# Optimization experiments

Measured on AMD Instinct MI355X. Metric: run time of the kernel, lower is better.

Reference implementation:

```python
import jax, jax.numpy as jnp
import numpy as np

IN_F = 4096
OUT_F = 8192
BLOCK = 16   # block_dim
KEEP = 8     # keep_k low-frequency modes kept per block
NLEV = 256   # n_levels


def dct_inv_basis(keep_k, n):
    # Orthonormal DCT-II synthesis basis, rows = kept frequencies k, cols = time index t.
    k = jnp.arange(keep_k, dtype=jnp.float32)[:, None]
    t = jnp.arange(n, dtype=jnp.float32)[None, :]
    B = jnp.cos(jnp.pi * (t + 0.5) * k / n) * jnp.sqrt(2.0 / n)
    scale = jnp.where(jnp.arange(keep_k) == 0, 1.0 / jnp.sqrt(2.0), 1.0)
    return B * scale[:, None]  # [keep_k, block_dim]


def setup_inputs() -> dict:
    key = jax.random.key(0)
    k1, k2, k3, k4, k5 = jax.random.split(key, 5)
    n_blocks = OUT_F * IN_F // BLOCK  # 2097152
    x = jax.random.normal(k1, (32, 8, IN_F), jnp.float32)
    idx = jax.random.randint(k2, (n_blocks, KEEP), 0, NLEV, jnp.int32)
    c_min = jax.random.normal(k3, (KEEP,), jnp.float32)
    c_range = jax.random.uniform(k4, (KEEP,), jnp.float32) + 0.1
    bias = jax.random.normal(k5, (OUT_F,), jnp.float32)
    return {"x": x, "idx": idx, "c_min": c_min, "c_range": c_range, "bias": bias}


def reference(x, idx, c_min, c_range, bias):
    # Affine dequant of kept frequency codes: [n_blocks, keep_k]
    coeffs = idx.astype(jnp.float32) / (NLEV - 1) * c_range + c_min
    # Inverse DCT per block (high-frequency modes are implicitly zero)
    B = dct_inv_basis(KEEP, BLOCK)              # [keep_k, block_dim]
    W = (coeffs @ B).reshape(OUT_F, IN_F)       # dense dequantized weight
    return x @ W.T + bias
```

## Files before the change

### kernel.cpp

```cpp
#include <hip/hip_runtime.h>


typedef __attribute__((ext_vector_type(8))) short bf16x8;
typedef __attribute__((ext_vector_type(4))) float f32x4;

#define K_TOT  2048
#define N_TOT  8192
#define KSTEPS 64
#define DEPTH  4

__device__ __forceinline__ unsigned short f2bf_rn(float f) {
    unsigned u = __float_as_uint(f);
    u += 0x7FFFu + ((u >> 16) & 1u);
    return (unsigned short)(u >> 16);
}

__device__ __forceinline__ unsigned pack2(int a, int b) {
    unsigned ua = __float_as_uint((float)a);
    unsigned ub = __float_as_uint((float)b);
    return __builtin_amdgcn_perm(ub, ua, 0x07060302u);
}

__device__ __forceinline__ bf16x8 cvt_bfrag(int4 lo, int4 hi) {
    union { unsigned u[4]; bf16x8 v; } r;
    r.u[0] = pack2(lo.x, lo.y);
    r.u[1] = pack2(lo.z, lo.w);
    r.u[2] = pack2(hi.x, hi.y);
    r.u[3] = pack2(hi.z, hi.w);
    return r.v;
}

__global__ __launch_bounds__(256) void prep_kernel(
    const float* __restrict__ x, const float* __restrict__ c_min,
    const float* __restrict__ c_range, unsigned short* __restrict__ Y2f,
    float* __restrict__ corr)
{
    __shared__ float Bk[8][16];
    __shared__ float scmin[8];
    __shared__ float ss[8];
    __shared__ float red[4];
    const int tid = threadIdx.x;
    const int m = blockIdx.x;
    if (tid < 128) {
        int k = tid >> 4, t = tid & 15;
        float v = cosf(3.14159265358979f * (t + 0.5f) * (float)k / 16.0f)
                  * 0.353553390593274f;
        if (k == 0) v *= 0.707106781186548f;
        Bk[k][t] = v;
    }
    if (tid < 8) {
        scmin[tid] = c_min[tid];
        ss[tid] = c_range[tid] * (1.0f / 255.0f);
    }
    __syncthreads();

    const float* xp = x + (long)m * 4096 + tid * 16;
    float xs[16];
#pragma unroll
    for (int q = 0; q < 4; ++q) {
        float4 v = *(const float4*)(xp + q * 4);
        xs[q * 4 + 0] = v.x; xs[q * 4 + 1] = v.y;
        xs[q * 4 + 2] = v.z; xs[q * 4 + 3] = v.w;
    }
    float partial = 0.0f;
    unsigned short yo[8];
#pragma unroll
    for (int k = 0; k < 8; ++k) {
        float y = 0.0f;
#pragma unroll
        for (int t = 0; t < 16; ++t) y += xs[t] * Bk[k][t];
        partial += y * scmin[k];
        yo[k] = f2bf_rn(y * ss[k]);
    }
    uint4 pk;
    pk.x = (unsigned)yo[0] | ((unsigned)yo[1] << 16);
    pk.y = (unsigned)yo[2] | ((unsigned)yo[3] << 16);
    pk.z = (unsigned)yo[4] | ((unsigned)yo[5] << 16);
    pk.w = (unsigned)yo[6] | ((unsigned)yo[7] << 16);

    {
        const int mg = m >> 4, fr = m & 15, kc = tid >> 2, fq = tid & 3;
        unsigned short* dst = Y2f + ((long)((mg * 64 + kc) * 64) + fq * 16 + fr) * 8;
        *(uint4*)dst = pk;
    }

#pragma unroll
    for (int off = 32; off > 0; off >>= 1)
        partial += __shfl_down(partial, off, 64);
    if ((tid & 63) == 0) red[tid >> 6] = partial;
    __syncthreads();
    if (tid == 0) corr[m] = red[0] + red[1] + red[2] + red[3];
}

__global__ __launch_bounds__(256, 2) void gemm_kernel(
    const unsigned short* __restrict__ Y2f, const int* __restrict__ idx,
    const float* __restrict__ bias, const float* __restrict__ corr,
    float* __restrict__ out)
{
    const int tid  = threadIdx.x;
    const int wave = tid >> 6;
    const int lane = tid & 63;
    const int fr   = lane & 15;
    const int fq   = lane >> 4;
    const int o0   = blockIdx.x * 16;

    const int* bPtr = idx + (long)(o0 + fr) * K_TOT + fq * 8;
    const unsigned short* aPtr = Y2f + ((long)(wave * 4) * KSTEPS * 64 + lane) * 8;

    int4 bLo[DEPTH], bHi[DEPTH];
    bf16x8 aF[2][4];
    f32x4 acc[4] = {{0.f,0.f,0.f,0.f},{0.f,0.f,0.f,0.f},
                    {0.f,0.f,0.f,0.f},{0.f,0.f,0.f,0.f}};

#pragma unroll
    for (int s = 0; s < DEPTH; ++s) {
        const int* p = bPtr + s * 32;
        bLo[s] = *(const int4*)p;
        bHi[s] = *(const int4*)(p + 4);
    }
#pragma unroll
    for (int mt = 0; mt < 4; ++mt) {
        aF[0][mt] = *(const bf16x8*)(aPtr + mt * 32768);
        aF[1][mt] = *(const bf16x8*)(aPtr + mt * 32768 + 512);
    }

    for (int kc = 0; kc < KSTEPS; kc += DEPTH) {
#pragma unroll
        for (int u = 0; u < DEPTH; ++u) {
            const int k = kc + u;
            bf16x8 bf = cvt_bfrag(bLo[u], bHi[u]);
            if (k + DEPTH < KSTEPS) {
                const int* p = bPtr + (k + DEPTH) * 32;
                bLo[u] = *(const int4*)p;
                bHi[u] = *(const int4*)(p + 4);
            }
#pragma unroll
            for (int mt = 0; mt < 4; ++mt)
                acc[mt] = __builtin_amdgcn_mfma_f32_16x16x32_bf16(
                    aF[k & 1][mt], bf, acc[mt], 0, 0, 0);
            if (k + 2 < KSTEPS) {
#pragma unroll
                for (int mt = 0; mt < 4; ++mt)
                    aF[k & 1][mt] =
                        *(const bf16x8*)(aPtr + mt * 32768 + (k + 2) * 512);
            }
        }
    }

    const int col = o0 + fr;
    const float bv = bias[col];
#pragma unroll
    for (int mt = 0; mt < 4; ++mt) {
        const int row0 = wave * 64 + mt * 16 + fq * 4;
#pragma unroll
        for (int r = 0; r < 4; ++r)
            out[(long)(row0 + r) * N_TOT + col] = acc[mt][r] + bv + corr[row0 + r];
    }
}

extern "C" void kernel_launch(void* const* d_in, const int* in_sizes, int n_in,
                              void* d_out, int out_size, void* d_ws, size_t ws_size,
                              hipStream_t stream) {
    const float* x       = (const float*)d_in[0];
    const int*   idx     = (const int*)d_in[1];
    const float* c_min   = (const float*)d_in[2];
    const float* c_range = (const float*)d_in[3];
    const float* bias    = (const float*)d_in[4];
    float* out = (float*)d_out;

    unsigned short* Y2f = (unsigned short*)d_ws;
    float* corr = (float*)((char*)d_ws + (size_t)256 * K_TOT * 2);

    prep_kernel<<<256, 256, 0, stream>>>(x, c_min, c_range, Y2f, corr);
    gemm_kernel<<<N_TOT / 16, 256, 0, stream>>>(Y2f, idx, bias, corr, out);
}
```

Measured before the change: 148.6 us.

## Stage idx codes through double-buffered LDS with coalesced loads and wider output tiles

The GEMM kernel now has 512-thread blocks, each covering 32 output columns. The int32 idx codes are loaded with coalesced row-contiguous loads, converted to bf16 and written into a double-buffered LDS layout matched to the MFMA fragments. Each wave now computes 2x2 MFMA tiles over 32 rows rather than 4 tiles over 64 rows. The goal is better global-load coalescing on the dominant 64MB idx stream and register-level reuse of A and B fragments. The cost is LDS barriers every chunk and more total A-fragment reads.

Result: faster. 125.8 us (-15.3%).

```diff
diff --git a/kernel.cpp b/kernel.cpp
--- a/kernel.cpp
+++ b/kernel.cpp
@@ -4,30 +4,29 @@
 typedef __attribute__((ext_vector_type(8))) short bf16x8;
 typedef __attribute__((ext_vector_type(4))) float f32x4;
 
-#define K_TOT  2048
-#define N_TOT  8192
-#define KSTEPS 64
-#define DEPTH  4
+#define K_TOT   2048
+#define N_TOT   8192
+#define NT      32
+#define NCHUNK  8
+#define SPC     8
+#define LDS_CH  16384
 
 __device__ __forceinline__ unsigned short f2bf_rn(float f) {
     unsigned u = __float_as_uint(f);
     u += 0x7FFFu + ((u >> 16) & 1u);
     return (unsigned short)(u >> 16);
 }
-
 __device__ __forceinline__ unsigned pack2(int a, int b) {
     unsigned ua = __float_as_uint((float)a);
     unsigned ub = __float_as_uint((float)b);
     return __builtin_amdgcn_perm(ub, ua, 0x07060302u);
 }
 
-__device__ __forceinline__ bf16x8 cvt_bfrag(int4 lo, int4 hi) {
-    union { unsigned u[4]; bf16x8 v; } r;
-    r.u[0] = pack2(lo.x, lo.y);
-    r.u[1] = pack2(lo.z, lo.w);
-    r.u[2] = pack2(hi.x, hi.y);
-    r.u[3] = pack2(hi.z, hi.w);
-    return r.v;
+__device__ __forceinline__ void lds_barrier() {
+    asm volatile("" ::: "memory");
+    __builtin_amdgcn_s_waitcnt(0xC07F);
+    __builtin_amdgcn_s_barrier();
+    asm volatile("" ::: "memory");
 }
 
 __global__ __launch_bounds__(256) void prep_kernel(
@@ -77,13 +76,11 @@
     pk.y = (unsigned)yo[2] | ((unsigned)yo[3] << 16);
     pk.z = (unsigned)yo[4] | ((unsigned)yo[5] << 16);
     pk.w = (unsigned)yo[6] | ((unsigned)yo[7] << 16);
-
     {
         const int mg = m >> 4, fr = m & 15, kc = tid >> 2, fq = tid & 3;
         unsigned short* dst = Y2f + ((long)((mg * 64 + kc) * 64) + fq * 16 + fr) * 8;
         *(uint4*)dst = pk;
     }
-
 #pragma unroll
     for (int off = 32; off > 0; off >>= 1)
         partial += __shfl_down(partial, off, 64);
@@ -92,70 +89,118 @@
     if (tid == 0) corr[m] = red[0] + red[1] + red[2] + red[3];
 }
 
-__global__ __launch_bounds__(256, 2) void gemm_kernel(
+struct Stage { int4 v[4]; };
+
+__global__ __launch_bounds__(512, 2) void gemm_kernel(
     const unsigned short* __restrict__ Y2f, const int* __restrict__ idx,
     const float* __restrict__ bias, const float* __restrict__ corr,
     float* __restrict__ out)
 {
+    __shared__ char lds[2 * LDS_CH];
+
     const int tid  = threadIdx.x;
     const int wave = tid >> 6;
     const int lane = tid & 63;
     const int fr   = lane & 15;
     const int fq   = lane >> 4;
-    const int o0   = blockIdx.x * 16;
-
-    const int* bPtr = idx + (long)(o0 + fr) * K_TOT + fq * 8;
-    const unsigned short* aPtr = Y2f + ((long)(wave * 4) * KSTEPS * 64 + lane) * 8;
-
-    int4 bLo[DEPTH], bHi[DEPTH];
-    bf16x8 aF[2][4];
-    f32x4 acc[4] = {{0.f,0.f,0.f,0.f},{0.f,0.f,0.f,0.f},
-                    {0.f,0.f,0.f,0.f},{0.f,0.f,0.f,0.f}};
-
-#pragma unroll
-    for (int s = 0; s < DEPTH; ++s) {
-        const int* p = bPtr + s * 32;
-        bLo[s] = *(const int4*)p;
-        bHi[s] = *(const int4*)(p + 4);
-    }
-#pragma unroll
-    for (int mt = 0; mt < 4; ++mt) {
-        aF[0][mt] = *(const bf16x8*)(aPtr + mt * 32768);
-        aF[1][mt] = *(const bf16x8*)(aPtr + mt * 32768 + 512);
-    }
-
-    for (int kc = 0; kc < KSTEPS; kc += DEPTH) {
-#pragma unroll
-        for (int u = 0; u < DEPTH; ++u) {
-            const int k = kc + u;
-            bf16x8 bf = cvt_bfrag(bLo[u], bHi[u]);
-            if (k + DEPTH < KSTEPS) {
-                const int* p = bPtr + (k + DEPTH) * 32;
-                bLo[u] = *(const int4*)p;
-                bHi[u] = *(const int4*)(p + 4);
-            }
-#pragma unroll
-            for (int mt = 0; mt < 4; ++mt)
-                acc[mt] = __builtin_amdgcn_mfma_f32_16x16x32_bf16(
-                    aF[k & 1][mt], bf, acc[mt], 0, 0, 0);
-            if (k + 2 < KSTEPS) {
-#pragma unroll
-                for (int mt = 0; mt < 4; ++mt)
-                    aF[k & 1][mt] =
-                        *(const bf16x8*)(aPtr + mt * 32768 + (k + 2) * 512);
+    const int o0   = blockIdx.x * NT;
+
+    const int* sBase = idx + (long)(o0 + wave) * K_TOT + lane * 4;
+    const int dstBase = (((lane >> 3) * 4 + ((lane & 7) >> 1)) * 32 + wave) * 16
+                        + (lane & 1) * 8;
+
+    const bf16x8* aB[2];
+    aB[0] = (const bf16x8*)Y2f + (long)((wave * 2 + 0) * 64) * 64 + lane;
+    aB[1] = (const bf16x8*)Y2f + (long)((wave * 2 + 1) * 64) * 64 + lane;
+
+    f32x4 acc[2][2] = {{{0.f,0.f,0.f,0.f},{0.f,0.f,0.f,0.f}},
+                       {{0.f,0.f,0.f,0.f},{0.f,0.f,0.f,0.f}}};
+
+    Stage S[2];
+
+#define STAGE_LOAD(slot, ch)                                              \
+    {                                                                     \
+        _Pragma("unroll")                                                 \
+        for (int l = 0; l < 4; ++l)                                       \
+            S[slot].v[l] = *(const int4*)(sBase + l * 8 * K_TOT + (ch) * 256); \
+    }
+
+#define STAGE_WRITE(slot, ch)                                             \
+    {                                                                     \
+        char* buf = lds + ((ch) & 1) * LDS_CH;                            \
+        _Pragma("unroll")                                                 \
+        for (int l = 0; l < 4; ++l) {                                     \
+            uint2 w;                                                      \
+            w.x = pack2(S[slot].v[l].x, S[slot].v[l].y);                  \
+            w.y = pack2(S[slot].v[l].z, S[slot].v[l].w);                  \
+            *(uint2*)(buf + dstBase + l * 128) = w;                       \
+        }                                                                 \
+    }
+
+#define COMPUTE(ch)                                                       \
+    {                                                                     \
+        const char* buf = lds + ((ch) & 1) * LDS_CH;                      \
+        bf16x8 a[SPC][2];                                                 \
+        _Pragma("unroll")                                                 \
+        for (int s = 0; s < SPC; ++s) {                                   \
+            a[s][0] = aB[0][((ch) * SPC + s) * 64];                       \
+            a[s][1] = aB[1][((ch) * SPC + s) * 64];                       \
+        }                                                                 \
+        bf16x8 b[2][2];                                                   \
+        _Pragma("unroll")                                                 \
+        for (int g = 0; g < 2; ++g)                                       \
+            b[0][g] = *(const bf16x8*)(buf + ((0 * 4 + fq) * 32 + g * 16 + fr) * 16); \
+        _Pragma("unroll")                                                 \
+        for (int s = 0; s < SPC; ++s) {                                   \
+            if (s + 1 < SPC) {                                            \
+                _Pragma("unroll")                                         \
+                for (int g = 0; g < 2; ++g)                               \
+                    b[(s + 1) & 1][g] = *(const bf16x8*)(buf +            \
+                        (((s + 1) * 4 + fq) * 32 + g * 16 + fr) * 16);    \
+            }                                                             \
+            _Pragma("unroll")                                             \
+            for (int mt = 0; mt < 2; ++mt) {                              \
+                _Pragma("unroll")                                         \
+                for (int g = 0; g < 2; ++g)                               \
+                    acc[mt][g] = __builtin_amdgcn_mfma_f32_16x16x32_bf16( \
+                        a[s][mt], b[s & 1][g], acc[mt][g], 0, 0, 0);      \
+            }                                                             \
+        }                                                                 \
+    }
+
+    STAGE_LOAD(0, 0)
+    STAGE_LOAD(1, 1)
+    STAGE_WRITE(0, 0)
+    lds_barrier();
+
+#pragma unroll
+    for (int c = 0; c < NCHUNK - 2; ++c) {
+        COMPUTE(c)
+        STAGE_LOAD(c & 1, c + 2)
+        STAGE_WRITE((c + 1) & 1, c + 1)
+        lds_barrier();
+    }
+    COMPUTE(NCHUNK - 2)
+    STAGE_WRITE((NCHUNK - 1) & 1, NCHUNK - 1)
+    lds_barrier();
+    COMPUTE(NCHUNK - 1)
+
+#pragma unroll
+    for (int mt = 0; mt < 2; ++mt) {
+#pragma unroll
+        for (int g = 0; g < 2; ++g) {
+            const int col = o0 + g * 16 + fr;
+            const float bv = bias[col];
+#pragma unroll
+            for (int r = 0; r < 4; ++r) {
+                const int row = (wave * 2 + mt) * 16 + fq * 4 + r;
+                out[(long)row * N_TOT + col] = acc[mt][g][r] + bv + corr[row];
             }
         }
     }
-
-    const int col = o0 + fr;
-    const float bv = bias[col];
-#pragma unroll
-    for (int mt = 0; mt < 4; ++mt) {
-        const int row0 = wave * 64 + mt * 16 + fq * 4;
-#pragma unroll
-        for (int r = 0; r < 4; ++r)
-            out[(long)(row0 + r) * N_TOT + col] = acc[mt][r] + bv + corr[row0 + r];
-    }
+#undef STAGE_LOAD
+#undef STAGE_WRITE
+#undef COMPUTE
 }
 
 extern "C" void kernel_launch(void* const* d_in, const int* in_sizes, int n_in,
@@ -172,5 +217,5 @@
     float* corr = (float*)((char*)d_ws + (size_t)256 * K_TOT * 2);
 
     prep_kernel<<<256, 256, 0, stream>>>(x, c_min, c_range, Y2f, corr);
-    gemm_kernel<<<N_TOT / 16, 256, 0, stream>>>(Y2f, idx, bias, corr, out);
-}
+    gemm_kernel<<<N_TOT / NT, 512, 0, stream>>>(Y2f, idx, bias, corr, out);
+}
```

## Use 2x2 MFMA tiles per wave with 512-thread blocks and deeper prefetch

Applied to the files above, without the earlier changes.

The GEMM kernel now gives each block 32 output columns and 8 waves, and each wave computes a 32x32 tile as a 2x2 grid of 16x16 MFMA tiles. Before, each wave did 64x16 as four tiles in a row. The idx prefetch depth grows from 4 to 8 k-steps and the activation prefetch from 2 to 4, using volatile vector loads so the loads issue in program order. The goal is more memory-level parallelism on the streamed int32 idx codes, with each B fragment reused across two M tiles. The cost is more registers per thread, 8 waves per block re-reading the same idx rows through cache, and volatile loads that stop the compiler from merging or rescheduling them.

Result: slower. 277.3 us (+86.7%).

```diff
diff --git a/kernel.cpp b/kernel.cpp
--- a/kernel.cpp
+++ b/kernel.cpp
@@ -1,33 +1,33 @@
 #include <hip/hip_runtime.h>
 
 
+typedef int v4i __attribute__((ext_vector_type(4)));
 typedef __attribute__((ext_vector_type(8))) short bf16x8;
 typedef __attribute__((ext_vector_type(4))) float f32x4;
 
-#define K_TOT  2048
-#define N_TOT  8192
-#define KSTEPS 64
-#define DEPTH  4
+#define K_TOT   2048
+#define N_TOT   8192
 
 __device__ __forceinline__ unsigned short f2bf_rn(float f) {
     unsigned u = __float_as_uint(f);
     u += 0x7FFFu + ((u >> 16) & 1u);
     return (unsigned short)(u >> 16);
 }
-
-__device__ __forceinline__ unsigned pack2(int a, int b) {
+__device__ __forceinline__ unsigned pk2(int a, int b) {
     unsigned ua = __float_as_uint((float)a);
     unsigned ub = __float_as_uint((float)b);
     return __builtin_amdgcn_perm(ub, ua, 0x07060302u);
 }
-
-__device__ __forceinline__ bf16x8 cvt_bfrag(int4 lo, int4 hi) {
+__device__ __forceinline__ bf16x8 cvt8(v4i lo, v4i hi) {
     union { unsigned u[4]; bf16x8 v; } r;
-    r.u[0] = pack2(lo.x, lo.y);
-    r.u[1] = pack2(lo.z, lo.w);
-    r.u[2] = pack2(hi.x, hi.y);
-    r.u[3] = pack2(hi.z, hi.w);
+    r.u[0] = pk2(lo[0], lo[1]);
+    r.u[1] = pk2(lo[2], lo[3]);
+    r.u[2] = pk2(hi[0], hi[1]);
+    r.u[3] = pk2(hi[2], hi[3]);
     return r.v;
+}
+__device__ __forceinline__ bf16x8 as_bf(v4i v) {
+    union { v4i i; bf16x8 b; } u; u.i = v; return u.b;
 }
 
 __global__ __launch_bounds__(256) void prep_kernel(
@@ -72,18 +72,16 @@
         partial += y * scmin[k];
         yo[k] = f2bf_rn(y * ss[k]);
     }
-    uint4 pk;
-    pk.x = (unsigned)yo[0] | ((unsigned)yo[1] << 16);
-    pk.y = (unsigned)yo[2] | ((unsigned)yo[3] << 16);
-    pk.z = (unsigned)yo[4] | ((unsigned)yo[5] << 16);
-    pk.w = (unsigned)yo[6] | ((unsigned)yo[7] << 16);
-
+    uint4 pkv;
+    pkv.x = (unsigned)yo[0] | ((unsigned)yo[1] << 16);
+    pkv.y = (unsigned)yo[2] | ((unsigned)yo[3] << 16);
+    pkv.z = (unsigned)yo[4] | ((unsigned)yo[5] << 16);
+    pkv.w = (unsigned)yo[6] | ((unsigned)yo[7] << 16);
     {
         const int mg = m >> 4, fr = m & 15, kc = tid >> 2, fq = tid & 3;
         unsigned short* dst = Y2f + ((long)((mg * 64 + kc) * 64) + fq * 16 + fr) * 8;
-        *(uint4*)dst = pk;
-    }
-
+        *(uint4*)dst = pkv;
+    }
 #pragma unroll
     for (int off = 32; off > 0; off >>= 1)
         partial += __shfl_down(partial, off, 64);
@@ -92,7 +90,9 @@
     if (tid == 0) corr[m] = red[0] + red[1] + red[2] + red[3];
 }
 
-__global__ __launch_bounds__(256, 2) void gemm_kernel(
+#define VL(p, o) (*((const volatile v4i*)(p) + (o)))
+
+__global__ __launch_bounds__(512, 2) void gemm_kernel(
     const unsigned short* __restrict__ Y2f, const int* __restrict__ idx,
     const float* __restrict__ bias, const float* __restrict__ corr,
     float* __restrict__ out)
@@ -102,59 +102,83 @@
     const int lane = tid & 63;
     const int fr   = lane & 15;
     const int fq   = lane >> 4;
-    const int o0   = blockIdx.x * 16;
-
-    const int* bPtr = idx + (long)(o0 + fr) * K_TOT + fq * 8;
-    const unsigned short* aPtr = Y2f + ((long)(wave * 4) * KSTEPS * 64 + lane) * 8;
-
-    int4 bLo[DEPTH], bHi[DEPTH];
-    bf16x8 aF[2][4];
-    f32x4 acc[4] = {{0.f,0.f,0.f,0.f},{0.f,0.f,0.f,0.f},
-                    {0.f,0.f,0.f,0.f},{0.f,0.f,0.f,0.f}};
-
-#pragma unroll
-    for (int s = 0; s < DEPTH; ++s) {
-        const int* p = bPtr + s * 32;
-        bLo[s] = *(const int4*)p;
-        bHi[s] = *(const int4*)(p + 4);
-    }
-#pragma unroll
-    for (int mt = 0; mt < 4; ++mt) {
-        aF[0][mt] = *(const bf16x8*)(aPtr + mt * 32768);
-        aF[1][mt] = *(const bf16x8*)(aPtr + mt * 32768 + 512);
-    }
-
-    for (int kc = 0; kc < KSTEPS; kc += DEPTH) {
-#pragma unroll
-        for (int u = 0; u < DEPTH; ++u) {
-            const int k = kc + u;
-            bf16x8 bf = cvt_bfrag(bLo[u], bHi[u]);
-            if (k + DEPTH < KSTEPS) {
-                const int* p = bPtr + (k + DEPTH) * 32;
-                bLo[u] = *(const int4*)p;
-                bHi[u] = *(const int4*)(p + 4);
-            }
-#pragma unroll
-            for (int mt = 0; mt < 4; ++mt)
-                acc[mt] = __builtin_amdgcn_mfma_f32_16x16x32_bf16(
-                    aF[k & 1][mt], bf, acc[mt], 0, 0, 0);
-            if (k + 2 < KSTEPS) {
-#pragma unroll
-                for (int mt = 0; mt < 4; ++mt)
-                    aF[k & 1][mt] =
-                        *(const bf16x8*)(aPtr + mt * 32768 + (k + 2) * 512);
-            }
+    const int o0   = blockIdx.x * 32;
+
+    const v4i* b0 = (const v4i*)(idx + (long)(o0 + fr) * K_TOT + fq * 8);
+    const v4i* b1 = (const v4i*)(idx + (long)(o0 + 16 + fr) * K_TOT + fq * 8);
+    const v4i* a0 = (const v4i*)((const char*)Y2f + (long)(wave * 2 + 0) * 65536 + lane * 16);
+    const v4i* a1 = (const v4i*)((const char*)Y2f + (long)(wave * 2 + 1) * 65536 + lane * 16);
+
+    v4i B[8][4];
+    v4i A[4][2];
+
+#pragma unroll
+    for (int s = 0; s < 8; ++s) {
+        B[s][0] = VL(b0, s * 8);     B[s][1] = VL(b0, s * 8 + 1);
+        B[s][2] = VL(b1, s * 8);     B[s][3] = VL(b1, s * 8 + 1);
+    }
+#pragma unroll
+    for (int d = 0; d < 4; ++d) {
+        A[d][0] = VL(a0, d * 64);    A[d][1] = VL(a1, d * 64);
+    }
+
+    f32x4 acc[2][2];
+#pragma unroll
+    for (int mt = 0; mt < 2; ++mt)
+#pragma unroll
+        for (int g = 0; g < 2; ++g)
+            acc[mt][g] = (f32x4){0.f, 0.f, 0.f, 0.f};
+
+    const v4i* b0c = b0; const v4i* b1c = b1;
+    const v4i* a0c = a0; const v4i* a1c = a1;
+
+    for (int kk = 0; kk < 7; ++kk) {
+#pragma unroll
+        for (int s = 0; s < 8; ++s) {
+            bf16x8 bf0 = cvt8(B[s][0], B[s][1]);
+            bf16x8 bf1 = cvt8(B[s][2], B[s][3]);
+            bf16x8 af0 = as_bf(A[s & 3][0]);
+            bf16x8 af1 = as_bf(A[s & 3][1]);
+            acc[0][0] = __builtin_amdgcn_mfma_f32_16x16x32_bf16(af0, bf0, acc[0][0], 0, 0, 0);
+            acc[1][0] = __builtin_amdgcn_mfma_f32_16x16x32_bf16(af1, bf0, acc[1][0], 0, 0, 0);
+            acc[0][1] = __builtin_amdgcn_mfma_f32_16x16x32_bf16(af0, bf1, acc[0][1], 0, 0, 0);
+            acc[1][1] = __builtin_amdgcn_mfma_f32_16x16x32_bf16(af1, bf1, acc[1][1], 0, 0, 0);
+            B[s][0] = VL(b0c, (s + 8) * 8);     B[s][1] = VL(b0c, (s + 8) * 8 + 1);
+            B[s][2] = VL(b1c, (s + 8) * 8);     B[s][3] = VL(b1c, (s + 8) * 8 + 1);
+            A[s & 3][0] = VL(a0c, (s + 4) * 64);
+            A[s & 3][1] = VL(a1c, (s + 4) * 64);
         }
-    }
-
-    const int col = o0 + fr;
-    const float bv = bias[col];
-#pragma unroll
-    for (int mt = 0; mt < 4; ++mt) {
-        const int row0 = wave * 64 + mt * 16 + fq * 4;
-#pragma unroll
-        for (int r = 0; r < 4; ++r)
-            out[(long)(row0 + r) * N_TOT + col] = acc[mt][r] + bv + corr[row0 + r];
+        b0c += 64; b1c += 64;
+        a0c += 512; a1c += 512;
+    }
+#pragma unroll
+    for (int s = 0; s < 8; ++s) {
+        bf16x8 bf0 = cvt8(B[s][0], B[s][1]);
+        bf16x8 bf1 = cvt8(B[s][2], B[s][3]);
+        bf16x8 af0 = as_bf(A[s & 3][0]);
+        bf16x8 af1 = as_bf(A[s & 3][1]);
+        acc[0][0] = __builtin_amdgcn_mfma_f32_16x16x32_bf16(af0, bf0, acc[0][0], 0, 0, 0);
+        acc[1][0] = __builtin_amdgcn_mfma_f32_16x16x32_bf16(af1, bf0, acc[1][0], 0, 0, 0);
+        acc[0][1] = __builtin_amdgcn_mfma_f32_16x16x32_bf16(af0, bf1, acc[0][1], 0, 0, 0);
+        acc[1][1] = __builtin_amdgcn_mfma_f32_16x16x32_bf16(af1, bf1, acc[1][1], 0, 0, 0);
+        if (s < 4) {
+            A[s & 3][0] = VL(a0c, (s + 4) * 64);
+            A[s & 3][1] = VL(a1c, (s + 4) * 64);
+        }
+    }
+
+#pragma unroll
+    for (int mt = 0; mt < 2; ++mt) {
+        const int row0 = (wave * 2 + mt) * 16 + fq * 4;
+#pragma unroll
+        for (int g = 0; g < 2; ++g) {
+            const int col = o0 + g * 16 + fr;
+            const float bv = bias[col];
+#pragma unroll
+            for (int r = 0; r < 4; ++r)
+                out[(long)(row0 + r) * N_TOT + col] =
+                    acc[mt][g][r] + bv + corr[row0 + r];
+        }
     }
 }
 
@@ -172,5 +196,5 @@
     float* corr = (float*)((char*)d_ws + (size_t)256 * K_TOT * 2);
 
     prep_kernel<<<256, 256, 0, stream>>>(x, c_min, c_range, Y2f, corr);
-    gemm_kernel<<<N_TOT / 16, 256, 0, stream>>>(Y2f, idx, bias, corr, out);
-}
+    gemm_kernel<<<N_TOT / 32, 512, 0, stream>>>(Y2f, idx, bias, corr, out);
+}
```
